# Optimization experiments

Hardware: AMD Instinct MI355X
Metric: run time of the kernel (lower is better)

## Reference

```python
import jax, jax.numpy as jnp
import numpy as np

B, S, E, H = 8, 2048, 1024, 128  # batch, seq, emd_dim, head_size
DROP_P = 0.1


def setup_inputs() -> dict:
    key = jax.random.key(0)
    kx, ku, kq, kk, kv = jax.random.split(key, 5)
    x = jax.random.normal(kx, (B, S, E), dtype=jnp.float32)
    drop_u = jax.random.uniform(ku, (B, S, S), dtype=jnp.float32)
    # Linear(emd_dim, head_size, bias=False): store weights as [E, H] so y = x @ W
    scale = 1.0 / np.sqrt(E)
    wq = jax.random.uniform(kq, (E, H), dtype=jnp.float32, minval=-scale, maxval=scale)
    wk = jax.random.uniform(kk, (E, H), dtype=jnp.float32, minval=-scale, maxval=scale)
    wv = jax.random.uniform(kv, (E, H), dtype=jnp.float32, minval=-scale, maxval=scale)
    return {"x": x, "wq": wq, "wk": wk, "wv": wv, "drop_u": drop_u}


def reference(x, wq, wk, wv, drop_u):
    Edim = x.shape[-1]
    q = x @ wq  # [B,S,H]
    k = x @ wk
    v = x @ wv
    # NOTE: module scales by emd_dim**-0.5 (E), not head_size**-0.5
    att = jnp.einsum("bsh,bth->bst", q, k) * (Edim ** -0.5)
    att = jax.nn.softmax(att, axis=-1)
    # deterministic inverted dropout with p=0.1
    keep = (drop_u >= DROP_P).astype(att.dtype) / (1.0 - DROP_P)
    att = att * keep
    return jnp.einsum("bst,bth->bsh", att, v)
```

## Files before the change

kernel.cpp:

```cpp
#include <hip/hip_runtime.h>
#include <hip/hip_bf16.h>
#include <stdint.h>
#include <stddef.h>

#define B_ 8
#define S_ 2048
#define E_ 1024
#define H_ 128
#define NR_ (B_ * S_)

typedef __attribute__((ext_vector_type(8))) short short8;
typedef __attribute__((ext_vector_type(4))) float f32x4;

__device__ __forceinline__ short f2bf(float f){
  uint32_t u = __builtin_bit_cast(uint32_t, f);
  u = (u + 0x7FFFu + ((u >> 16) & 1u)) >> 16;
  return (short)(uint16_t)u;
}

#define GLOBAL_AS __attribute__((address_space(1)))
#define LDS_AS    __attribute__((address_space(3)))
__device__ __forceinline__ void async16(const void* g, void* l){
  __builtin_amdgcn_global_load_lds((const GLOBAL_AS uint32_t*)g,
                                   (LDS_AS uint32_t*)l, 16, 0, 0);
}

__global__ void cast_x(const float* __restrict__ x, short* __restrict__ xb){
  size_t i = ((size_t)blockIdx.x * 256 + threadIdx.x) * 8;
  f32x4 a = *(const f32x4*)(x + i);
  f32x4 b = *(const f32x4*)(x + i + 4);
  short8 o;
#pragma unroll
  for (int j = 0; j < 4; j++){ o[j] = f2bf(a[j]); o[j + 4] = f2bf(b[j]); }
  *(short8*)(xb + i) = o;
}

__global__ void pack_w(const float* __restrict__ wq, const float* __restrict__ wk,
                       const float* __restrict__ wv, short* __restrict__ wt){
  __shared__ float t[32][33];
  int idx = blockIdx.x;
  int hb  = idx & 3;
  int eb  = (idx >> 2) & 31;
  int w   = idx >> 7;
  const float* src = (w == 0) ? wq : (w == 1) ? wk : wv;
  int c  = threadIdx.x & 31;
  int r0 = threadIdx.x >> 5;
#pragma unroll
  for (int i = 0; i < 4; i++){
    int r = r0 * 4 + i;
    t[r][c] = src[(size_t)(eb * 32 + r) * H_ + hb * 32 + c];
  }
  __syncthreads();
#pragma unroll
  for (int i = 0; i < 4; i++){
    int r = r0 * 4 + i;
    wt[(size_t)(w * 128 + hb * 32 + r) * E_ + eb * 32 + c] = f2bf(t[c][r]);
  }
}

__launch_bounds__(256)
__global__ void qkv_gemm(const short* __restrict__ xb, const short* __restrict__ wt,
                         short* __restrict__ qm, short* __restrict__ km,
                         short* __restrict__ vtmp){
  __shared__ __align__(16) short abuf[2][4096];
  __shared__ __align__(16) short bbuf[2][4096];
  const int wave = threadIdx.x >> 6;
  const int lane = threadIdx.x & 63;
  const int l16  = lane & 15;
  const int quad = lane >> 4;
  const int nb   = blockIdx.x;
  const int m0   = blockIdx.y * 128;
  const int n0   = nb * 128;

  f32x4 acc[4][4];
#pragma unroll
  for (int i = 0; i < 4; i++)
#pragma unroll
    for (int j = 0; j < 4; j++) acc[i][j] = (f32x4)(0.0f);

#define STAGE(buf, k0)                                                        \
  {                                                                           \
    _Pragma("unroll")                                                         \
    for (int i = 0; i < 2; i++){                                              \
      int c = wave * 2 + i;                                                   \
      int r = c * 16 + (lane >> 2);                                           \
      int q = ((lane & 3) ^ ((r >> 1) & 3)) & 3;                              \
      async16(xb + (size_t)(m0 + r) * E_ + (k0) + q * 8,                      \
              (char*)abuf[buf] + c * 1024);                                   \
      async16(wt + (size_t)(n0 + r) * E_ + (k0) + q * 8,                      \
              (char*)bbuf[buf] + c * 1024);                                   \
    }                                                                         \
  }

  STAGE(0, 0)
  for (int ks = 0; ks < 32; ks++){
    const int k0 = ks * 32;
    __syncthreads();
    if (ks < 31) STAGE((ks + 1) & 1, k0 + 32)

    const short* ab = abuf[ks & 1];
    const short* bb = bbuf[ks & 1];
    short8 af[4], bf[4];
#pragma unroll
    for (int t = 0; t < 4; t++){
      int ra = (wave & 1) * 64 + t * 16 + l16;
      int pa = (quad ^ ((ra >> 1) & 3)) & 3;
      af[t] = *(const short8*)(ab + ra * 32 + pa * 8);
      int rb = (wave >> 1) * 64 + t * 16 + l16;
      int pb = (quad ^ ((rb >> 1) & 3)) & 3;
      bf[t] = *(const short8*)(bb + rb * 32 + pb * 8);
    }
#pragma unroll
    for (int mt = 0; mt < 4; mt++)
#pragma unroll
      for (int nt = 0; nt < 4; nt++)
        acc[mt][nt] = __builtin_amdgcn_mfma_f32_16x16x32_bf16(af[mt], bf[nt], acc[mt][nt], 0, 0, 0);
  }
#undef STAGE

  short* dst = (nb == 0) ? qm : (nb == 1) ? km : vtmp;
#pragma unroll
  for (int mt = 0; mt < 4; mt++)
#pragma unroll
    for (int nt = 0; nt < 4; nt++){
      int row = m0 + (wave & 1) * 64 + mt * 16 + quad * 4;
      int col = (wave >> 1) * 64 + nt * 16 + l16;
#pragma unroll
      for (int r = 0; r < 4; r++)
        dst[(size_t)(row + r) * H_ + col] = f2bf(acc[mt][nt][r]);
    }
}

__global__ void transpose_v(const short* __restrict__ v, short* __restrict__ vt){
  __shared__ short t[32][33];
  int idx = blockIdx.x;
  int hb = idx & 3;
  int sb = (idx >> 2) & 63;
  int b  = idx >> 8;
  int s0 = sb * 32, h0 = hb * 32;
  int c  = threadIdx.x & 31;
  int r0 = threadIdx.x >> 5;
#pragma unroll
  for (int i = 0; i < 4; i++){
    int r = r0 * 4 + i;
    t[r][c] = v[((size_t)b * S_ + s0 + r) * H_ + h0 + c];
  }
  __syncthreads();
#pragma unroll
  for (int i = 0; i < 4; i++){
    int r = r0 * 4 + i;
    vt[((size_t)b * H_ + h0 + r) * S_ + s0 + c] = t[c][r];
  }
}

__launch_bounds__(256)
__global__ void attn(const short* __restrict__ qm, const short* __restrict__ km,
                     const short* __restrict__ vtm, const float* __restrict__ du,
                     float* __restrict__ po, float* __restrict__ pl,
                     float* __restrict__ out, int split){
  const int wave = threadIdx.x >> 6;
  const int lane = threadIdx.x & 63;
  const int l16  = lane & 15;
  const int quad = lane >> 4;
  const int sp   = blockIdx.x & (split - 1);
  const int rbk  = blockIdx.x / split;
  const int b    = rbk >> 5;
  const int m0   = (rbk & 31) * 64 + wave * 16;
  const int seg  = S_ / split;

  const short* qb  = qm  + ((size_t)b * S_ + m0) * H_;
  const short* kb  = km  + (size_t)b * S_ * H_;
  const short* vb  = vtm + (size_t)b * H_ * S_;
  const float* dub = du  + ((size_t)b * S_ + m0) * S_;

  __shared__ __align__(16) short kls[8192];
  __shared__ __align__(16) short vls[8192];
  __shared__ float pbuf[4][16][68];
  float* pb = &pbuf[wave][0][0];

  short8 qf[4];
#pragma unroll
  for (int kc = 0; kc < 4; kc++)
    qf[kc] = *(const short8*)(qb + (size_t)l16 * H_ + kc * 32 + quad * 8);

  f32x4 o[8];
#pragma unroll
  for (int ht = 0; ht < 8; ht++) o[ht] = (f32x4)(0.0f);
  float lpart[4] = {0.f, 0.f, 0.f, 0.f};

  const float SC2  = 0.045084220f;
  const float KINV = 1.0f / 0.9f;

  const int tbeg = sp * seg;
  for (int t0 = tbeg; t0 < tbeg + seg; t0 += 64){
#pragma unroll
    for (int i = 0; i < 4; i++){
      int c = wave * 4 + i;
      int r = c * 4 + (lane >> 4);
      int s = lane & 15;
      int q = (s & 8) | ((s ^ r) & 7);
      async16(kb + (size_t)(t0 + r) * H_ + q * 8, (char*)kls + c * 1024);
    }
#pragma unroll
    for (int i = 0; i < 4; i++){
      int c = wave * 4 + i;
      int r = c * 8 + (lane >> 3);
      int s = lane & 7;
      int q = (s ^ r) & 7;
      async16(vb + (size_t)r * S_ + t0 + q * 8, (char*)vls + c * 1024);
    }
    __syncthreads();

    const float* dp = dub + (size_t)l16 * S_ + t0 + quad * 8;
    f32x4 u0 = *(const f32x4*)(dp);
    f32x4 u1 = *(const f32x4*)(dp + 4);
    f32x4 u2 = *(const f32x4*)(dp + 32);
    f32x4 u3 = *(const f32x4*)(dp + 36);

    f32x4 s[4];
#pragma unroll
    for (int nt = 0; nt < 4; nt++) s[nt] = (f32x4)(0.0f);
#pragma unroll
    for (int nt = 0; nt < 4; nt++){
      int row = nt * 16 + l16;
#pragma unroll
      for (int kc = 0; kc < 4; kc++){
        int q  = kc * 4 + quad;
        int ph = (q & 8) | ((q ^ row) & 7);
        short8 bf = *(const short8*)((const char*)kls + row * 256 + ph * 16);
        s[nt] = __builtin_amdgcn_mfma_f32_16x16x32_bf16(qf[kc], bf, s[nt], 0, 0, 0);
      }
    }

#pragma unroll
    for (int nt = 0; nt < 4; nt++)
#pragma unroll
      for (int r = 0; r < 4; r++){
        float p = exp2f(s[nt][r] * SC2);
        lpart[r] += p;
        pb[(quad * 4 + r) * 68 + nt * 16 + l16] = p;
      }

    __builtin_amdgcn_sched_barrier(0);
    __builtin_amdgcn_s_waitcnt(0xC07F);
    __builtin_amdgcn_sched_barrier(0);

    const float* pr = pb + l16 * 68 + quad * 8;
    f32x4 p0 = *(const f32x4*)(pr);
    f32x4 p1 = *(const f32x4*)(pr + 4);
    f32x4 p2 = *(const f32x4*)(pr + 32);
    f32x4 p3 = *(const f32x4*)(pr + 36);
    short8 pa0, pa1;
#pragma unroll
    for (int j = 0; j < 4; j++){
      pa0[j]     = f2bf((u0[j] >= 0.1f) ? p0[j] * KINV : 0.0f);
      pa0[j + 4] = f2bf((u1[j] >= 0.1f) ? p1[j] * KINV : 0.0f);
      pa1[j]     = f2bf((u2[j] >= 0.1f) ? p2[j] * KINV : 0.0f);
      pa1[j + 4] = f2bf((u3[j] >= 0.1f) ? p3[j] * KINV : 0.0f);
    }

#pragma unroll
    for (int ht = 0; ht < 8; ht++){
      int row = ht * 16 + l16;
#pragma unroll
      for (int half = 0; half < 2; half++){
        int q  = half * 4 + quad;
        int ph = (q ^ row) & 7;
        short8 vf = *(const short8*)((const char*)vls + row * 128 + ph * 16);
        o[ht] = __builtin_amdgcn_mfma_f32_16x16x32_bf16(half ? pa1 : pa0, vf, o[ht], 0, 0, 0);
      }
    }
    __syncthreads();
  }

  float lrow[4];
#pragma unroll
  for (int r = 0; r < 4; r++){
    float v = lpart[r];
    v += __shfl_xor(v, 1);
    v += __shfl_xor(v, 2);
    v += __shfl_xor(v, 4);
    v += __shfl_xor(v, 8);
    lrow[r] = v;
  }

  if (split == 1){
    float* op = out + ((size_t)b * S_ + m0) * H_;
#pragma unroll
    for (int ht = 0; ht < 8; ht++)
#pragma unroll
      for (int r = 0; r < 4; r++)
        op[(size_t)(quad * 4 + r) * H_ + ht * 16 + l16] = o[ht][r] / lrow[r];
  } else {
#pragma unroll
    for (int r = 0; r < 4; r++){
      size_t R = (size_t)b * S_ + m0 + quad * 4 + r;
#pragma unroll
      for (int ht = 0; ht < 8; ht++)
        po[((size_t)sp * NR_ + R) * H_ + ht * 16 + l16] = o[ht][r];
      if (l16 == 0) pl[(size_t)sp * NR_ + R] = lrow[r];
    }
  }
}

__global__ void combine(const float* __restrict__ po, const float* __restrict__ pl,
                        float* __restrict__ out, int split){
  int row = blockIdx.x;
  int col = threadIdx.x;
  float num = 0.f, den = 0.f;
  for (int s = 0; s < split; s++){
    num += po[((size_t)s * NR_ + row) * H_ + col];
    den += pl[(size_t)s * NR_ + row];
  }
  out[(size_t)row * H_ + col] = num / den;
}

extern "C" void kernel_launch(void* const* d_in, const int* in_sizes, int n_in,
                              void* d_out, int out_size, void* d_ws, size_t ws_size,
                              hipStream_t stream){
  const float* x  = (const float*)d_in[0];
  const float* wq = (const float*)d_in[1];
  const float* wk = (const float*)d_in[2];
  const float* wv = (const float*)d_in[3];
  const float* du = (const float*)d_in[4];
  float* out = (float*)d_out;

  const size_t MiB = 1048576;
  char* ws = (char*)d_ws;
  short* qm = (short*)(ws);
  short* km = (short*)(ws + 4 * MiB);
  short* vt = (short*)(ws + 8 * MiB);

  size_t needA = (size_t)(76.5 * MiB);
  size_t needB = (size_t)(60.5 * MiB);
  int split;
  float *pl = nullptr, *po = nullptr;
  short *wt, *vtmp, *xb;
  if (ws_size >= needA){
    split = 4;
    pl   = (float*)(ws + 12 * MiB);
    po   = (float*)(ws + 12 * MiB + 524288);
    wt   = (short*)(ws + 12 * MiB + 524288);
    vtmp = (short*)(ws + 12 * MiB + 524288 + 1 * MiB);
    xb   = (short*)(ws + 12 * MiB + 524288 + 32 * MiB);
  } else if (ws_size >= needB){
    split = 2;
    pl   = (float*)(ws + 12 * MiB);
    po   = (float*)(ws + 12 * MiB + 524288);
    wt   = (short*)(ws + 12 * MiB + 524288);
    vtmp = (short*)(ws + 12 * MiB + 524288 + 1 * MiB);
    xb   = (short*)(ws + 12 * MiB + 524288 + 16 * MiB);
  } else {
    split = 1;
    xb   = (short*)(ws + 8 * MiB);
    wt   = (short*)(ws + 40 * MiB);
    vtmp = (short*)(ws + 40 * MiB + 786432);
  }

  hipLaunchKernelGGL(cast_x,      dim3(8192),      dim3(256), 0, stream, x, xb);
  hipLaunchKernelGGL(pack_w,      dim3(384),       dim3(256), 0, stream, wq, wk, wv, wt);
  hipLaunchKernelGGL(qkv_gemm,    dim3(3, 128),    dim3(256), 0, stream, xb, wt, qm, km, vtmp);
  hipLaunchKernelGGL(transpose_v, dim3(2048),      dim3(256), 0, stream, vtmp, vt);
  hipLaunchKernelGGL(attn,        dim3(256 * split), dim3(256), 0, stream,
                     qm, km, vt, du, po, pl, out, split);
  if (split > 1)
    hipLaunchKernelGGL(combine, dim3(NR_), dim3(H_), 0, stream, po, pl, out, split);
}
```

Before: 302.1 us.

## Fuse prep kernels, transpose V in GEMM epilogue, widen attention blocks

Merges the x cast and weight packing into one launch, and writes V transposed straight from the QKV GEMM epilogue through LDS, which removes the separate transpose kernel and its round trip through memory. The attention kernel moves to 512-thread blocks covering 128 query rows, so each K/V tile loaded into LDS is shared by twice as many waves. Probabilities are staged in LDS as bf16 instead of fp32, and the 1/0.9 dropout scale is applied once at output. This lowers launch overhead and memory traffic, at the cost of a lower grid count, more LDS per block and a small precision change in the staged probabilities.

```diff
diff --git a/kernel.cpp b/kernel.cpp
--- a/kernel.cpp
+++ b/kernel.cpp
@@ -10,6 +10,7 @@
 #define NR_ (B_ * S_)
 
 typedef __attribute__((ext_vector_type(8))) short short8;
+typedef __attribute__((ext_vector_type(4))) short short4v;
 typedef __attribute__((ext_vector_type(4))) float f32x4;
 
 __device__ __forceinline__ short f2bf(float f){
@@ -25,45 +26,46 @@
                                    (LDS_AS uint32_t*)l, 16, 0, 0);
 }
 
-__global__ void cast_x(const float* __restrict__ x, short* __restrict__ xb){
-  size_t i = ((size_t)blockIdx.x * 256 + threadIdx.x) * 8;
-  f32x4 a = *(const f32x4*)(x + i);
-  f32x4 b = *(const f32x4*)(x + i + 4);
-  short8 o;
-#pragma unroll
-  for (int j = 0; j < 4; j++){ o[j] = f2bf(a[j]); o[j + 4] = f2bf(b[j]); }
-  *(short8*)(xb + i) = o;
-}
-
-__global__ void pack_w(const float* __restrict__ wq, const float* __restrict__ wk,
-                       const float* __restrict__ wv, short* __restrict__ wt){
+__global__ void prep(const float* __restrict__ x, const float* __restrict__ wq,
+                     const float* __restrict__ wk, const float* __restrict__ wv,
+                     short* __restrict__ xb, short* __restrict__ wt){
   __shared__ float t[32][33];
-  int idx = blockIdx.x;
-  int hb  = idx & 3;
-  int eb  = (idx >> 2) & 31;
-  int w   = idx >> 7;
-  const float* src = (w == 0) ? wq : (w == 1) ? wk : wv;
-  int c  = threadIdx.x & 31;
-  int r0 = threadIdx.x >> 5;
-#pragma unroll
-  for (int i = 0; i < 4; i++){
-    int r = r0 * 4 + i;
-    t[r][c] = src[(size_t)(eb * 32 + r) * H_ + hb * 32 + c];
-  }
-  __syncthreads();
-#pragma unroll
-  for (int i = 0; i < 4; i++){
-    int r = r0 * 4 + i;
-    wt[(size_t)(w * 128 + hb * 32 + r) * E_ + eb * 32 + c] = f2bf(t[c][r]);
+  int bid = blockIdx.x;
+  if (bid < 8192){
+    size_t i = ((size_t)bid * 256 + threadIdx.x) * 8;
+    f32x4 a = *(const f32x4*)(x + i);
+    f32x4 b = *(const f32x4*)(x + i + 4);
+    short8 o;
+#pragma unroll
+    for (int j = 0; j < 4; j++){ o[j] = f2bf(a[j]); o[j + 4] = f2bf(b[j]); }
+    *(short8*)(xb + i) = o;
+  } else {
+    int idx = bid - 8192;
+    int hb  = idx & 3;
+    int eb  = (idx >> 2) & 31;
+    int w   = idx >> 7;
+    const float* src = (w == 0) ? wq : (w == 1) ? wk : wv;
+    int c  = threadIdx.x & 31;
+    int r0 = threadIdx.x >> 5;
+#pragma unroll
+    for (int i = 0; i < 4; i++){
+      int r = r0 * 4 + i;
+      t[r][c] = src[(size_t)(eb * 32 + r) * H_ + hb * 32 + c];
+    }
+    __syncthreads();
+#pragma unroll
+    for (int i = 0; i < 4; i++){
+      int r = r0 * 4 + i;
+      wt[(size_t)(w * 128 + hb * 32 + r) * E_ + eb * 32 + c] = f2bf(t[c][r]);
+    }
   }
 }
 
 __launch_bounds__(256)
 __global__ void qkv_gemm(const short* __restrict__ xb, const short* __restrict__ wt,
                          short* __restrict__ qm, short* __restrict__ km,
-                         short* __restrict__ vtmp){
-  __shared__ __align__(16) short abuf[2][4096];
-  __shared__ __align__(16) short bbuf[2][4096];
+                         short* __restrict__ vt){
+  __shared__ __align__(16) short smem[16896];
   const int wave = threadIdx.x >> 6;
   const int lane = threadIdx.x & 63;
   const int l16  = lane & 15;
@@ -86,9 +88,9 @@
       int r = c * 16 + (lane >> 2);                                           \
       int q = ((lane & 3) ^ ((r >> 1) & 3)) & 3;                              \
       async16(xb + (size_t)(m0 + r) * E_ + (k0) + q * 8,                      \
-              (char*)abuf[buf] + c * 1024);                                   \
+              (char*)(smem + (buf) * 4096) + c * 1024);                       \
       async16(wt + (size_t)(n0 + r) * E_ + (k0) + q * 8,                      \
-              (char*)bbuf[buf] + c * 1024);                                   \
+              (char*)(smem + 8192 + (buf) * 4096) + c * 1024);                \
     }                                                                         \
   }
 
@@ -98,17 +100,17 @@
     __syncthreads();
     if (ks < 31) STAGE((ks + 1) & 1, k0 + 32)
 
-    const short* ab = abuf[ks & 1];
-    const short* bb = bbuf[ks & 1];
+    const short* a = smem + (ks & 1) * 4096;
+    const short* b = smem + 8192 + (ks & 1) * 4096;
     short8 af[4], bf[4];
 #pragma unroll
     for (int t = 0; t < 4; t++){
       int ra = (wave & 1) * 64 + t * 16 + l16;
       int pa = (quad ^ ((ra >> 1) & 3)) & 3;
-      af[t] = *(const short8*)(ab + ra * 32 + pa * 8);
+      af[t] = *(const short8*)(a + ra * 32 + pa * 8);
       int rb = (wave >> 1) * 64 + t * 16 + l16;
       int pb = (quad ^ ((rb >> 1) & 3)) & 3;
-      bf[t] = *(const short8*)(bb + rb * 32 + pb * 8);
+      bf[t] = *(const short8*)(b + rb * 32 + pb * 8);
     }
 #pragma unroll
     for (int mt = 0; mt < 4; mt++)
@@ -118,42 +120,44 @@
   }
 #undef STAGE
 
-  short* dst = (nb == 0) ? qm : (nb == 1) ? km : vtmp;
-#pragma unroll
-  for (int mt = 0; mt < 4; mt++)
-#pragma unroll
-    for (int nt = 0; nt < 4; nt++){
-      int row = m0 + (wave & 1) * 64 + mt * 16 + quad * 4;
-      int col = (wave >> 1) * 64 + nt * 16 + l16;
-#pragma unroll
-      for (int r = 0; r < 4; r++)
-        dst[(size_t)(row + r) * H_ + col] = f2bf(acc[mt][nt][r]);
-    }
-}
-
-__global__ void transpose_v(const short* __restrict__ v, short* __restrict__ vt){
-  __shared__ short t[32][33];
-  int idx = blockIdx.x;
-  int hb = idx & 3;
-  int sb = (idx >> 2) & 63;
-  int b  = idx >> 8;
-  int s0 = sb * 32, h0 = hb * 32;
-  int c  = threadIdx.x & 31;
-  int r0 = threadIdx.x >> 5;
-#pragma unroll
-  for (int i = 0; i < 4; i++){
-    int r = r0 * 4 + i;
-    t[r][c] = v[((size_t)b * S_ + s0 + r) * H_ + h0 + c];
-  }
-  __syncthreads();
-#pragma unroll
-  for (int i = 0; i < 4; i++){
-    int r = r0 * 4 + i;
-    vt[((size_t)b * H_ + h0 + r) * S_ + s0 + c] = t[c][r];
-  }
-}
-
-__launch_bounds__(256)
+  if (nb != 2){
+    short* dst = (nb == 0) ? qm : km;
+#pragma unroll
+    for (int mt = 0; mt < 4; mt++)
+#pragma unroll
+      for (int nt = 0; nt < 4; nt++){
+        int row = m0 + (wave & 1) * 64 + mt * 16 + quad * 4;
+        int col = (wave >> 1) * 64 + nt * 16 + l16;
+#pragma unroll
+        for (int r = 0; r < 4; r++)
+          dst[(size_t)(row + r) * H_ + col] = f2bf(acc[mt][nt][r]);
+      }
+  } else {
+    __syncthreads();
+#pragma unroll
+    for (int mt = 0; mt < 4; mt++)
+#pragma unroll
+      for (int nt = 0; nt < 4; nt++){
+        int scol = (wave & 1) * 64 + mt * 16 + quad * 4;
+        int hrow = (wave >> 1) * 64 + nt * 16 + l16;
+        short4v t4;
+#pragma unroll
+        for (int r = 0; r < 4; r++) t4[r] = f2bf(acc[mt][nt][r]);
+        *(short4v*)(smem + hrow * 132 + scol) = t4;
+      }
+    __syncthreads();
+    int h   = threadIdx.x >> 1;
+    int s0  = (threadIdx.x & 1) * 64;
+    int bb_ = m0 >> 11;
+    short* dstv = vt + ((size_t)bb_ * H_ + h) * S_ + (m0 & (S_ - 1)) + s0;
+    const short* srcv = smem + h * 132 + s0;
+#pragma unroll
+    for (int i = 0; i < 8; i++)
+      *(short8*)(dstv + i * 8) = *(const short8*)(srcv + i * 8);
+  }
+}
+
+__launch_bounds__(512)
 __global__ void attn(const short* __restrict__ qm, const short* __restrict__ km,
                      const short* __restrict__ vtm, const float* __restrict__ du,
                      float* __restrict__ po, float* __restrict__ pl,
@@ -164,8 +168,8 @@
   const int quad = lane >> 4;
   const int sp   = blockIdx.x & (split - 1);
   const int rbk  = blockIdx.x / split;
-  const int b    = rbk >> 5;
-  const int m0   = (rbk & 31) * 64 + wave * 16;
+  const int b    = rbk >> 4;
+  const int m0   = (rbk & 15) * 128 + wave * 16;
   const int seg  = S_ / split;
 
   const short* qb  = qm  + ((size_t)b * S_ + m0) * H_;
@@ -175,8 +179,8 @@
 
   __shared__ __align__(16) short kls[8192];
   __shared__ __align__(16) short vls[8192];
-  __shared__ float pbuf[4][16][68];
-  float* pb = &pbuf[wave][0][0];
+  __shared__ short pbuf[8][16][72];
+  short* pb = &pbuf[wave][0][0];
 
   short8 qf[4];
 #pragma unroll
@@ -194,16 +198,16 @@
   const int tbeg = sp * seg;
   for (int t0 = tbeg; t0 < tbeg + seg; t0 += 64){
 #pragma unroll
-    for (int i = 0; i < 4; i++){
-      int c = wave * 4 + i;
+    for (int i = 0; i < 2; i++){
+      int c = wave * 2 + i;
       int r = c * 4 + (lane >> 4);
       int s = lane & 15;
       int q = (s & 8) | ((s ^ r) & 7);
       async16(kb + (size_t)(t0 + r) * H_ + q * 8, (char*)kls + c * 1024);
     }
 #pragma unroll
-    for (int i = 0; i < 4; i++){
-      int c = wave * 4 + i;
+    for (int i = 0; i < 2; i++){
+      int c = wave * 2 + i;
       int r = c * 8 + (lane >> 3);
       int s = lane & 7;
       int q = (s ^ r) & 7;
@@ -238,25 +242,23 @@
       for (int r = 0; r < 4; r++){
         float p = exp2f(s[nt][r] * SC2);
         lpart[r] += p;
-        pb[(quad * 4 + r) * 68 + nt * 16 + l16] = p;
+        pb[(quad * 4 + r) * 72 + nt * 16 + l16] = f2bf(p);
       }
 
     __builtin_amdgcn_sched_barrier(0);
     __builtin_amdgcn_s_waitcnt(0xC07F);
     __builtin_amdgcn_sched_barrier(0);
 
-    const float* pr = pb + l16 * 68 + quad * 8;
-    f32x4 p0 = *(const f32x4*)(pr);
-    f32x4 p1 = *(const f32x4*)(pr + 4);
-    f32x4 p2 = *(const f32x4*)(pr + 32);
-    f32x4 p3 = *(const f32x4*)(pr + 36);
+    const short* pr = pb + l16 * 72 + quad * 8;
+    short8 pb0 = *(const short8*)(pr);
+    short8 pb1 = *(const short8*)(pr + 32);
     short8 pa0, pa1;
 #pragma unroll
     for (int j = 0; j < 4; j++){
-      pa0[j]     = f2bf((u0[j] >= 0.1f) ? p0[j] * KINV : 0.0f);
-      pa0[j + 4] = f2bf((u1[j] >= 0.1f) ? p1[j] * KINV : 0.0f);
-      pa1[j]     = f2bf((u2[j] >= 0.1f) ? p2[j] * KINV : 0.0f);
-      pa1[j + 4] = f2bf((u3[j] >= 0.1f) ? p3[j] * KINV : 0.0f);
+      pa0[j]     = (u0[j] >= 0.1f) ? pb0[j]     : (short)0;
+      pa0[j + 4] = (u1[j] >= 0.1f) ? pb0[j + 4] : (short)0;
+      pa1[j]     = (u2[j] >= 0.1f) ? pb1[j]     : (short)0;
+      pa1[j + 4] = (u3[j] >= 0.1f) ? pb1[j + 4] : (short)0;
     }
 
 #pragma unroll
@@ -290,14 +292,14 @@
     for (int ht = 0; ht < 8; ht++)
 #pragma unroll
       for (int r = 0; r < 4; r++)
-        op[(size_t)(quad * 4 + r) * H_ + ht * 16 + l16] = o[ht][r] / lrow[r];
+        op[(size_t)(quad * 4 + r) * H_ + ht * 16 + l16] = o[ht][r] * KINV / lrow[r];
   } else {
 #pragma unroll
     for (int r = 0; r < 4; r++){
       size_t R = (size_t)b * S_ + m0 + quad * 4 + r;
 #pragma unroll
       for (int ht = 0; ht < 8; ht++)
-        po[((size_t)sp * NR_ + R) * H_ + ht * 16 + l16] = o[ht][r];
+        po[((size_t)sp * NR_ + R) * H_ + ht * 16 + l16] = o[ht][r] * KINV;
       if (l16 == 0) pl[(size_t)sp * NR_ + R] = lrow[r];
     }
   }
@@ -330,38 +332,19 @@
   short* qm = (short*)(ws);
   short* km = (short*)(ws + 4 * MiB);
   short* vt = (short*)(ws + 8 * MiB);
-
-  size_t needA = (size_t)(76.5 * MiB);
-  size_t needB = (size_t)(60.5 * MiB);
-  int split;
-  float *pl = nullptr, *po = nullptr;
-  short *wt, *vtmp, *xb;
-  if (ws_size >= needA){
-    split = 4;
-    pl   = (float*)(ws + 12 * MiB);
-    po   = (float*)(ws + 12 * MiB + 524288);
-    wt   = (short*)(ws + 12 * MiB + 524288);
-    vtmp = (short*)(ws + 12 * MiB + 524288 + 1 * MiB);
-    xb   = (short*)(ws + 12 * MiB + 524288 + 32 * MiB);
-  } else if (ws_size >= needB){
-    split = 2;
-    pl   = (float*)(ws + 12 * MiB);
-    po   = (float*)(ws + 12 * MiB + 524288);
-    wt   = (short*)(ws + 12 * MiB + 524288);
-    vtmp = (short*)(ws + 12 * MiB + 524288 + 1 * MiB);
-    xb   = (short*)(ws + 12 * MiB + 524288 + 16 * MiB);
-  } else {
-    split = 1;
-    xb   = (short*)(ws + 8 * MiB);
-    wt   = (short*)(ws + 40 * MiB);
-    vtmp = (short*)(ws + 40 * MiB + 786432);
-  }
-
-  hipLaunchKernelGGL(cast_x,      dim3(8192),      dim3(256), 0, stream, x, xb);
-  hipLaunchKernelGGL(pack_w,      dim3(384),       dim3(256), 0, stream, wq, wk, wv, wt);
-  hipLaunchKernelGGL(qkv_gemm,    dim3(3, 128),    dim3(256), 0, stream, xb, wt, qm, km, vtmp);
-  hipLaunchKernelGGL(transpose_v, dim3(2048),      dim3(256), 0, stream, vtmp, vt);
-  hipLaunchKernelGGL(attn,        dim3(256 * split), dim3(256), 0, stream,
+  short* xb = (short*)(ws + 12 * MiB);
+  short* wt = (short*)(ws + 44 * MiB);
+  float* pl = (float*)(ws + 45 * MiB);
+  float* po = (float*)(ws + 45 * MiB + 524288);
+
+  size_t base  = 45 * MiB + 524288;
+  size_t needA = base + 32 * MiB;
+  size_t needB = base + 16 * MiB;
+  int split = (ws_size >= needA) ? 4 : (ws_size >= needB) ? 2 : 1;
+
+  hipLaunchKernelGGL(prep,     dim3(8576),        dim3(256), 0, stream, x, wq, wk, wv, xb, wt);
+  hipLaunchKernelGGL(qkv_gemm, dim3(3, 128),      dim3(256), 0, stream, xb, wt, qm, km, vt);
+  hipLaunchKernelGGL(attn,     dim3(128 * split), dim3(512), 0, stream,
                      qm, km, vt, du, po, pl, out, split);
   if (split > 1)
     hipLaunchKernelGGL(combine, dim3(NR_), dim3(H_), 0, stream, po, pl, out, split);
```

New measurement: 290.7 us. -3.8%, faster.
